# Kernel optimization log

Hardware: AMD Instinct MI355X
Metric: run time of the kernel (lower is better)

The kernel has to match this reference:

```python
import jax, jax.numpy as jnp
import numpy as np

N = 16384      # nodes (256 chess boards x 64 squares)
E = 393216     # edges (avg degree 24)
G = 256        # graphs
HID = 128
H = 4
C = 32         # head dim
L = 8          # 4 blocks x 2 GATv2Conv
NODE_DIM = 21
EDGE_DIM = 6


def setup_inputs() -> dict:
    key = jax.random.key(0)
    ks = jax.random.split(key, 12)
    x = jax.random.normal(ks[0], (N, NODE_DIM), jnp.float32)
    edge_index = jax.random.randint(ks[1], (2, E), 0, N, dtype=jnp.int32)
    edge_attr = jax.random.uniform(ks[2], (E, EDGE_DIM), dtype=jnp.float32)
    batch = jnp.sort(jax.random.randint(ks[3], (N,), 0, G, dtype=jnp.int32))

    def w(k, shape, fan_in):
        return jax.random.normal(k, shape, jnp.float32) * (1.0 / np.sqrt(fan_in))

    Win = w(ks[4], (NODE_DIM, HID), NODE_DIM)
    b_in = jnp.zeros((HID,), jnp.float32)
    Wl = w(ks[5], (L, HID, HID), HID)
    bl = jnp.zeros((L, HID), jnp.float32)
    Wr = w(ks[6], (L, HID, HID), HID)
    br = jnp.zeros((L, HID), jnp.float32)
    We = w(ks[7], (L, EDGE_DIM, HID), EDGE_DIM)
    att = w(ks[8], (L, H, C), C)
    bconv = jnp.zeros((L, HID), jnp.float32)
    gamma = jnp.ones((L, HID), jnp.float32)
    beta = jnp.zeros((L, HID), jnp.float32)
    W1 = w(ks[9], (HID, 64), HID)
    b1 = jnp.zeros((64,), jnp.float32)
    W2 = w(ks[10], (64, 3), 64)
    b2 = jnp.zeros((3,), jnp.float32)
    return dict(x=x, edge_index=edge_index, edge_attr=edge_attr, batch=batch,
                Win=Win, b_in=b_in, Wl=Wl, bl=bl, Wr=Wr, br=br, We=We, att=att,
                bconv=bconv, gamma=gamma, beta=beta, W1=W1, b1=b1, W2=W2, b2=b2)


def _gatv2(h, src, dst, ea, Wl, bl, Wr, br, We, att, bias):
    # PyG GATv2Conv: message j->i uses x_j from lin_l, x_i from lin_r
    xl = (h @ Wl + bl).reshape(N, H, C)
    xr = (h @ Wr + br).reshape(N, H, C)
    ee = (ea @ We).reshape(-1, H, C)
    m = jax.nn.leaky_relu(xl[src] + xr[dst] + ee, 0.2)   # [Ef, H, C]
    s = jnp.einsum('ehc,hc->eh', m, att)                 # [Ef, H]
    smax = jax.ops.segment_max(s, dst, num_segments=N)   # self-loops => no empty segs
    ex = jnp.exp(s - smax[dst])
    den = jax.ops.segment_sum(ex, dst, num_segments=N)
    alpha = ex / den[dst]                                # edge softmax per target node
    out = jax.ops.segment_sum(alpha[:, :, None] * xl[src], dst, num_segments=N)
    return out.reshape(N, HID) + bias


def _bn(x, g, b):
    mu = jnp.mean(x, axis=0)
    var = jnp.var(x, axis=0)
    return g * (x - mu) * jax.lax.rsqrt(var + 1e-5) + b


def reference(x, edge_index, edge_attr, batch, Win, b_in, Wl, bl, Wr, br, We, att,
              bconv, gamma, beta, W1, b1, W2, b2):
    src0, dst0 = edge_index[0], edge_index[1]
    # add self-loops with fill_value='mean' (per-target mean of incoming edge_attr)
    deg = jax.ops.segment_sum(jnp.ones((E,), jnp.float32), dst0, num_segments=N)
    loop_attr = jax.ops.segment_sum(edge_attr, dst0, num_segments=N) / jnp.maximum(deg, 1.0)[:, None]
    idx = jnp.arange(N, dtype=src0.dtype)
    src = jnp.concatenate([src0, idx])
    dst = jnp.concatenate([dst0, idx])
    ea = jnp.concatenate([edge_attr, loop_attr], axis=0)

    h = jax.nn.relu(x @ Win + b_in)
    for blk in range(4):
        res = h
        l = 2 * blk
        h = jax.nn.relu(_bn(_gatv2(h, src, dst, ea, Wl[l], bl[l], Wr[l], br[l], We[l], att[l], bconv[l]), gamma[l], beta[l]))
        l = 2 * blk + 1
        h = _bn(_gatv2(h, src, dst, ea, Wl[l], bl[l], Wr[l], br[l], We[l], att[l], bconv[l]), gamma[l], beta[l])
        h = jax.nn.relu(h + res)

    cnt = jnp.maximum(jax.ops.segment_sum(jnp.ones((N,), jnp.float32), batch, num_segments=G), 1.0)
    pooled = jax.ops.segment_sum(h, batch, num_segments=G) / cnt[:, None]
    logits = jax.nn.relu(pooled @ W1 + b1) @ W2 + b2
    return logits
```

## Files before the change

kernel.cpp:

```cpp
#include <hip/hip_runtime.h>
#include <math.h>

constexpr int N   = 16384;
constexpr int E   = 393216;
constexpr int EF  = E + N;
constexpr int G   = 256;
constexpr int HID = 128;

__device__ __forceinline__ float red16(float x) {
    union fi { float f; int i; };
    fi a, b;
    a.f = x;
    b.i = __builtin_amdgcn_mov_dpp(a.i, 0x121, 0xf, 0xf, false); a.f += b.f;
    b.i = __builtin_amdgcn_mov_dpp(a.i, 0x122, 0xf, 0xf, false); a.f += b.f;
    b.i = __builtin_amdgcn_mov_dpp(a.i, 0x124, 0xf, 0xf, false); a.f += b.f;
    b.i = __builtin_amdgcn_mov_dpp(a.i, 0x128, 0xf, 0xf, false); a.f += b.f;
    return a.f;
}

__global__ __launch_bounds__(256) void k_hist(const int* __restrict__ dst,
                                              int* __restrict__ cnt) {
    int e = blockIdx.x * 256 + threadIdx.x;
    if (e < E) atomicAdd(&cnt[dst[e]], 1);
}

__global__ __launch_bounds__(1024) void k_scan(const int* __restrict__ cnt,
                                               int* __restrict__ row_ptr) {
    __shared__ int lds[1024];
    int t = threadIdx.x;
    int local[16];
    int s = 0;
    int base = t * 16;
#pragma unroll
    for (int q = 0; q < 16; q++) { local[q] = cnt[base + q] + 1; s += local[q]; }
    lds[t] = s;
    __syncthreads();
    for (int off = 1; off < 1024; off <<= 1) {
        int v = (t >= off) ? lds[t - off] : 0;
        __syncthreads();
        lds[t] += v;
        __syncthreads();
    }
    int run = (t == 0) ? 0 : lds[t - 1];
    if (t == 0) row_ptr[0] = 0;
#pragma unroll
    for (int q = 0; q < 16; q++) { run += local[q]; row_ptr[base + q + 1] = run; }
}

__global__ __launch_bounds__(256) void k_scatter(const int* __restrict__ src,
                                                 const int* __restrict__ dst,
                                                 const int* __restrict__ row_ptr,
                                                 int* __restrict__ cnt,
                                                 int* __restrict__ csr_src,
                                                 int* __restrict__ csr_eid) {
    int e = blockIdx.x * 256 + threadIdx.x;
    if (e >= E) return;
    int d = dst[e];
    int pos = row_ptr[d] + atomicSub(&cnt[d], 1) - 1;
    csr_src[pos] = src[e];
    csr_eid[pos] = e;
}

__global__ __launch_bounds__(256) void k_build_ea(const int* __restrict__ row_ptr,
                                                  int* __restrict__ csr_src,
                                                  int* __restrict__ csr_eid,
                                                  const float* __restrict__ edge_attr,
                                                  float* __restrict__ csr_ea) {
    int p = blockIdx.x * 256 + threadIdx.x;
    if (p < N) {
        int pos = row_ptr[p + 1] - 1;
        csr_src[pos] = p;
        csr_eid[pos] = E + p;
    }
    if (p >= EF) return;
    unsigned eid = (unsigned)csr_eid[p];
    if (eid >= (unsigned)E) return;
    const float* s = edge_attr + (size_t)eid * 6;
    float4 a = {s[0], s[1], s[2], s[3]};
    float4 b = {s[4], s[5], 0.0f, 0.0f};
    float4* dstp = (float4*)(csr_ea + (size_t)p * 8);
    dstp[0] = a;
    dstp[1] = b;
}

__global__ __launch_bounds__(256) void k_loopattr2(const int* __restrict__ row_ptr,
                                                   float* __restrict__ csr_ea) {
    int i = blockIdx.x * 256 + threadIdx.x;
    if (i >= N) return;
    int e0 = row_ptr[i], e1 = row_ptr[i + 1] - 1;
    float4 sa = {0, 0, 0, 0};
    float sbx = 0.0f, sby = 0.0f;
    for (int e = e0; e < e1; e++) {
        const float4* p = (const float4*)(csr_ea + (size_t)e * 8);
        float4 a = p[0];
        float4 b = p[1];
        sa.x += a.x; sa.y += a.y; sa.z += a.z; sa.w += a.w;
        sbx += b.x; sby += b.y;
    }
    float inv = 1.0f / fmaxf((float)(e1 - e0), 1.0f);
    float4 oa = {sa.x * inv, sa.y * inv, sa.z * inv, sa.w * inv};
    float4 ob = {sbx * inv, sby * inv, 0.0f, 0.0f};
    float4* q = (float4*)(csr_ea + (size_t)e1 * 8);
    q[0] = oa;
    q[1] = ob;
}

__global__ __launch_bounds__(128) void k_ingemm(const float* __restrict__ x,
                                                const float* __restrict__ Win,
                                                const float* __restrict__ b_in,
                                                float* __restrict__ h) {
    __shared__ float xs[21];
    int i = blockIdx.x;
    int c = threadIdx.x;
    if (c < 21) xs[c] = x[i * 21 + c];
    __syncthreads();
    float acc = b_in[c];
#pragma unroll
    for (int d = 0; d < 21; d++) acc += xs[d] * Win[d * HID + c];
    h[i * HID + c] = fmaxf(acc, 0.0f);
}

__global__ __launch_bounds__(256) void k_gemm_lr(const float* __restrict__ h,
                                                 const float* __restrict__ bns,
                                                 const float* __restrict__ gamma,
                                                 const float* __restrict__ beta,
                                                 float* __restrict__ res,
                                                 const float* __restrict__ Wl,
                                                 const float* __restrict__ bl,
                                                 const float* __restrict__ Wr,
                                                 const float* __restrict__ br,
                                                 float* __restrict__ XL,
                                                 float* __restrict__ XR) {
    __shared__ float hs[16][HID];
    __shared__ float sc[HID], sh[HID];
    int t = threadIdx.x;
    int r0 = blockIdx.x * 16;
    if (bns) {
        if (t < 128) {
            const float invN = 1.0f / (float)N;
            float mean = bns[t] * invN;
            float var  = bns[128 + t] * invN - mean * mean;
            float inv  = rsqrtf(var + 1e-5f);
            float s = gamma[t] * inv;
            sc[t] = s;
            sh[t] = beta[t] - mean * s;
        }
        __syncthreads();
    }
    {
        int row = t >> 4;
        int col = (t & 15) * 8;
        size_t base = (size_t)(r0 + row) * HID + col;
        const float4* src = (const float4*)&h[base];
        float4 a = src[0];
        float4 b = src[1];
        if (bns) {
            float4 s0 = *(const float4*)&sc[col];
            float4 s1 = *(const float4*)&sc[col + 4];
            float4 h0 = *(const float4*)&sh[col];
            float4 h1 = *(const float4*)&sh[col + 4];
            a.x = fmaf(a.x, s0.x, h0.x);
            a.y = fmaf(a.y, s0.y, h0.y);
            a.z = fmaf(a.z, s0.z, h0.z);
            a.w = fmaf(a.w, s0.w, h0.w);
            b.x = fmaf(b.x, s1.x, h1.x);
            b.y = fmaf(b.y, s1.y, h1.y);
            b.z = fmaf(b.z, s1.z, h1.z);
            b.w = fmaf(b.w, s1.w, h1.w);
            if (res) {
                const float4* rp = (const float4*)&res[base];
                float4 ra = rp[0];
                float4 rb = rp[1];
                a.x += ra.x; a.y += ra.y; a.z += ra.z; a.w += ra.w;
                b.x += rb.x; b.y += rb.y; b.z += rb.z; b.w += rb.w;
            }
            a.x = fmaxf(a.x, 0.0f); a.y = fmaxf(a.y, 0.0f);
            a.z = fmaxf(a.z, 0.0f); a.w = fmaxf(a.w, 0.0f);
            b.x = fmaxf(b.x, 0.0f); b.y = fmaxf(b.y, 0.0f);
            b.z = fmaxf(b.z, 0.0f); b.w = fmaxf(b.w, 0.0f);
            if (res) {
                float4* wp = (float4*)&res[base];
                wp[0] = a;
                wp[1] = b;
            }
        }
        float4* dst = (float4*)&hs[row][col];
        dst[0] = a;
        dst[1] = b;
    }
    __syncthreads();
    bool right = t >= 128;
    int cp = (t & 63) * 2;
    int rbase = ((t >> 6) & 1) * 8;
    const float* W    = right ? Wr : Wl;
    const float* bias = right ? br : bl;
    float* OUT        = right ? XR : XL;
    float b0 = bias[cp], b1 = bias[cp + 1];
    float acc0[8], acc1[8];
#pragma unroll
    for (int r = 0; r < 8; r++) { acc0[r] = b0; acc1[r] = b1; }
    for (int k = 0; k < HID; k += 4) {
        float4 h4[8];
#pragma unroll
        for (int r = 0; r < 8; r++) h4[r] = *(const float4*)&hs[rbase + r][k];
#pragma unroll
        for (int kk = 0; kk < 4; kk++) {
            float2 w = *(const float2*)&W[(size_t)(k + kk) * HID + cp];
#pragma unroll
            for (int r = 0; r < 8; r++) {
                float hv = ((const float*)&h4[r])[kk];
                acc0[r] = fmaf(hv, w.x, acc0[r]);
                acc1[r] = fmaf(hv, w.y, acc1[r]);
            }
        }
    }
#pragma unroll
    for (int r = 0; r < 8; r++) {
        float2 o = {acc0[r], acc1[r]};
        *(float2*)&OUT[(size_t)(r0 + rbase + r) * HID + cp] = o;
    }
}

__device__ __forceinline__ void pf_xl(int e, int e1,
                                      const int* __restrict__ csr_src,
                                      const float* __restrict__ xl, int ch0,
                                      float2 out[4]) {
#pragma unroll
    for (int k = 0; k < 4; k++) {
        int ec = (e + k < e1) ? e + k : e1 - 1;
        int j = __builtin_amdgcn_readfirstlane(csr_src[ec]);
        out[k] = *(const float2*)&xl[(size_t)j * HID + ch0];
    }
}

__global__ __launch_bounds__(1024) void k_edge(const int* __restrict__ row_ptr,
                                               const int* __restrict__ csr_src,
                                               const float* __restrict__ csr_ea,
                                               const float* __restrict__ xl,
                                               const float* __restrict__ xr,
                                               const float* __restrict__ We_l,
                                               const float* __restrict__ att_l,
                                               float* __restrict__ gout,
                                               float* __restrict__ bnsums) {
    __shared__ float red_lds[16][256];
    int w = threadIdx.x >> 6;
    int lane = threadIdx.x & 63;
    int hh = lane >> 4;
    int ss = lane & 15;
    int ch0 = hh * 32 + 2 * ss;
    int i = blockIdx.x * 16 + w;

    float a0 = att_l[ch0], a1 = att_l[ch0 + 1];
    float we0[6], we1[6];
#pragma unroll
    for (int d = 0; d < 6; d++) {
        float2 wv = *(const float2*)&We_l[d * HID + ch0];
        we0[d] = wv.x;
        we1[d] = wv.y;
    }

    float2 xr2 = *(const float2*)&xr[(size_t)i * HID + ch0];
    float rm = -INFINITY, rd = 0.0f, acc0 = 0.0f, acc1 = 0.0f;
    int e0 = __builtin_amdgcn_readfirstlane(row_ptr[i]);
    int e1 = __builtin_amdgcn_readfirstlane(row_ptr[i + 1]);

    auto body = [&](int e, const float2 xlv[4]) {
        float p[4];
#pragma unroll
        for (int k = 0; k < 4; k++) {
            int ee = e + k;
            int ec = (ee < e1) ? ee : (e1 - 1);
            const float4* ea4 = (const float4*)(csr_ea + (size_t)ec * 8);
            float4 eaA = ea4[0];
            float4 eaB = ea4[1];
            float u0 = eaA.x * we0[0], u1 = eaA.x * we1[0];
            u0 = fmaf(eaA.y, we0[1], u0); u1 = fmaf(eaA.y, we1[1], u1);
            u0 = fmaf(eaA.z, we0[2], u0); u1 = fmaf(eaA.z, we1[2], u1);
            u0 = fmaf(eaA.w, we0[3], u0); u1 = fmaf(eaA.w, we1[3], u1);
            u0 = fmaf(eaB.x, we0[4], u0); u1 = fmaf(eaB.x, we1[4], u1);
            u0 = fmaf(eaB.y, we0[5], u0); u1 = fmaf(eaB.y, we1[5], u1);
            float m0 = xlv[k].x + xr2.x + u0;
            float m1 = xlv[k].y + xr2.y + u1;
            m0 = fmaxf(m0, 0.2f * m0);
            m1 = fmaxf(m1, 0.2f * m1);
            float pv = m0 * a0;
            pv = fmaf(m1, a1, pv);
            pv = red16(pv);
            p[k] = (ee < e1) ? pv : -INFINITY;
        }
        float bm = fmaxf(fmaxf(p[0], p[1]), fmaxf(p[2], p[3]));
        float nm = fmaxf(rm, bm);
        float scal = __expf(rm - nm);
        rd *= scal; acc0 *= scal; acc1 *= scal;
#pragma unroll
        for (int k = 0; k < 4; k++) {
            float ek = __expf(p[k] - nm);
            rd += ek;
            acc0 = fmaf(ek, xlv[k].x, acc0);
            acc1 = fmaf(ek, xlv[k].y, acc1);
        }
        rm = nm;
    };

    float2 bufA[4], bufB[4];
    pf_xl(e0, e1, csr_src, xl, ch0, bufA);
    for (int e = e0; e < e1; e += 8) {
        pf_xl(e + 4, e1, csr_src, xl, ch0, bufB);
        body(e, bufA);
        pf_xl(e + 8, e1, csr_src, xl, ch0, bufA);
        if (e + 4 < e1) body(e + 4, bufB);
    }
    float inv = 1.0f / rd;
    float2 o = {acc0 * inv, acc1 * inv};
    *(float2*)&gout[(size_t)i * HID + ch0] = o;

    red_lds[w][ch0]       = o.x;
    red_lds[w][ch0 + 1]   = o.y;
    red_lds[w][128 + ch0]     = o.x * o.x;
    red_lds[w][128 + ch0 + 1] = o.y * o.y;
    __syncthreads();
    int t = threadIdx.x;
    if (t < 256) {
        float s = 0.0f;
#pragma unroll
        for (int q = 0; q < 16; q++) s += red_lds[q][t];
        atomicAdd(&bnsums[t], s);
    }
}

__global__ __launch_bounds__(128) void k_pool(const float* __restrict__ gout,
                                              const float* __restrict__ res,
                                              const float* __restrict__ bns,
                                              const float* __restrict__ gamma,
                                              const float* __restrict__ beta,
                                              const int* __restrict__ batch,
                                              const float* __restrict__ W1,
                                              const float* __restrict__ b1,
                                              const float* __restrict__ W2,
                                              const float* __restrict__ b2,
                                              float* __restrict__ out) {
    __shared__ float pooled[HID];
    __shared__ float hid[64];
    __shared__ int bounds[2];
    int g = blockIdx.x;
    int t = threadIdx.x;
    if (t < 2) {
        int target = g + t;
        int lo = 0, hi = N;
        while (lo < hi) {
            int mid = (lo + hi) >> 1;
            if (batch[mid] < target) lo = mid + 1; else hi = mid;
        }
        bounds[t] = lo;
    }
    const float invN = 1.0f / (float)N;
    float mean = bns[t] * invN;
    float var  = bns[128 + t] * invN - mean * mean;
    float scb  = gamma[t] * rsqrtf(var + 1e-5f);
    float shb  = beta[t] - mean * scb;
    __syncthreads();
    int s = bounds[0], e = bounds[1];
    float acc = 0.0f;
    for (int r = s; r < e; r++) {
        float v = fmaf(gout[(size_t)r * HID + t], scb, shb) + res[(size_t)r * HID + t];
        acc += fmaxf(v, 0.0f);
    }
    float cntf = fmaxf((float)(e - s), 1.0f);
    pooled[t] = acc / cntf;
    __syncthreads();
    if (t < 64) {
        float a = b1[t];
#pragma unroll 4
        for (int c = 0; c < HID; c++) a += pooled[c] * W1[c * 64 + t];
        hid[t] = fmaxf(a, 0.0f);
    }
    __syncthreads();
    if (t < 3) {
        float a = b2[t];
#pragma unroll
        for (int j = 0; j < 64; j++) a += hid[j] * W2[j * 3 + t];
        out[g * 3 + t] = a;
    }
}

extern "C" void kernel_launch(void* const* d_in, const int* in_sizes, int n_in,
                              void* d_out, int out_size, void* d_ws, size_t ws_size,
                              hipStream_t stream) {
    const float* x         = (const float*)d_in[0];
    const int*   edge_index= (const int*)d_in[1];
    const float* edge_attr = (const float*)d_in[2];
    const int*   batch     = (const int*)d_in[3];
    const float* Win       = (const float*)d_in[4];
    const float* b_in      = (const float*)d_in[5];
    const float* Wl        = (const float*)d_in[6];
    const float* bl        = (const float*)d_in[7];
    const float* Wr        = (const float*)d_in[8];
    const float* br        = (const float*)d_in[9];
    const float* We        = (const float*)d_in[10];
    const float* att       = (const float*)d_in[11];
    const float* gamma     = (const float*)d_in[13];
    const float* beta      = (const float*)d_in[14];
    const float* W1        = (const float*)d_in[15];
    const float* b1        = (const float*)d_in[16];
    const float* W2        = (const float*)d_in[17];
    const float* b2        = (const float*)d_in[18];
    float* out = (float*)d_out;

    const int* src0 = edge_index;
    const int* dst0 = edge_index + E;

    char* ws = (char*)d_ws;
    size_t off = 0;
    auto alloc = [&](size_t bytes) -> void* {
        void* p = ws + off;
        off += (bytes + 255) & ~(size_t)255;
        return p;
    };
    int*   cnt       = (int*)alloc((size_t)N * sizeof(int));
    float* bnsums    = (float*)alloc((size_t)8 * 256 * sizeof(float));
    int*   row_ptr   = (int*)alloc((size_t)(N + 1) * sizeof(int));
    int*   csr_src   = (int*)alloc((size_t)EF * sizeof(int));
    int*   csr_eid   = (int*)alloc((size_t)EF * sizeof(int));
    float* csr_ea    = (float*)alloc((size_t)EF * 8 * sizeof(float));
    float* H0        = (float*)alloc((size_t)N * HID * sizeof(float));
    float* XL        = (float*)alloc((size_t)N * HID * sizeof(float));
    float* XR        = (float*)alloc((size_t)N * HID * sizeof(float));
    float* GOUT      = (float*)alloc((size_t)N * HID * sizeof(float));

    size_t zbytes = (size_t)N * sizeof(int) + 8 * 256 * sizeof(float);
    hipMemsetAsync(cnt, 0, zbytes, stream);
    k_hist<<<(E + 255) / 256, 256, 0, stream>>>(dst0, cnt);
    k_scan<<<1, 1024, 0, stream>>>(cnt, row_ptr);
    k_scatter<<<(E + 255) / 256, 256, 0, stream>>>(src0, dst0, row_ptr, cnt,
                                                   csr_src, csr_eid);
    k_build_ea<<<(EF + 255) / 256, 256, 0, stream>>>(row_ptr, csr_src, csr_eid,
                                                     edge_attr, csr_ea);
    k_loopattr2<<<(N + 255) / 256, 256, 0, stream>>>(row_ptr, csr_ea);
    k_ingemm<<<N, 128, 0, stream>>>(x, Win, b_in, H0);

    for (int l = 0; l < 8; l++) {
        bool odd = (l & 1) != 0;
        const float* hin;
        const float* bns_in = nullptr;
        const float* g_in = nullptr;
        const float* b_in2 = nullptr;
        float* res = nullptr;
        if (l == 0) {
            hin = H0;
        } else {
            hin = GOUT;
            bns_in = bnsums + (l - 1) * 256;
            g_in  = gamma + (size_t)(l - 1) * HID;
            b_in2 = beta  + (size_t)(l - 1) * HID;
            if (!odd) res = H0;
        }
        k_gemm_lr<<<N / 16, 256, 0, stream>>>(hin, bns_in, g_in, b_in2, res,
                                              Wl + (size_t)l * HID * HID, bl + l * HID,
                                              Wr + (size_t)l * HID * HID, br + l * HID,
                                              XL, XR);
        k_edge<<<N / 16, 1024, 0, stream>>>(row_ptr, csr_src, csr_ea,
                                            XL, XR,
                                            We + (size_t)l * 6 * HID,
                                            att + (size_t)l * HID, GOUT,
                                            bnsums + l * 256);
    }
    k_pool<<<G, 128, 0, stream>>>(GOUT, H0, bnsums + 7 * 256,
                                  gamma + 7 * HID, beta + 7 * HID,
                                  batch, W1, b1, W2, b2, out);
}
```

Baseline: 737.7 us.

## Deepen edge-index prefetch, drop online-softmax max, fuse CSR attr build into scatter

The edge kernel now prefetches source indices three groups ahead, separately from the xl row gathers, so index-load latency is hidden behind the softmax body. The running-max online softmax is replaced with plain exp2 accumulation, with log2(e) folded into the attention weights. This removes the per-group max, rescale exponent and multiplies, but it no longer guards against overflow for large scores. Setup also drops k_build_ea and the csr_eid buffer by writing edge attributes directly in the scatter kernel, moves the self-loop index write into k_loopattr2, and adds an occupancy hint to the k_edge launch bounds.

```diff
diff --git a/kernel.cpp b/kernel.cpp
--- a/kernel.cpp
+++ b/kernel.cpp
@@ -51,39 +51,24 @@
                                                  const int* __restrict__ dst,
                                                  const int* __restrict__ row_ptr,
                                                  int* __restrict__ cnt,
+                                                 const float* __restrict__ edge_attr,
                                                  int* __restrict__ csr_src,
-                                                 int* __restrict__ csr_eid) {
+                                                 float* __restrict__ csr_ea) {
     int e = blockIdx.x * 256 + threadIdx.x;
     if (e >= E) return;
     int d = dst[e];
     int pos = row_ptr[d] + atomicSub(&cnt[d], 1) - 1;
     csr_src[pos] = src[e];
-    csr_eid[pos] = e;
-}
-
-__global__ __launch_bounds__(256) void k_build_ea(const int* __restrict__ row_ptr,
-                                                  int* __restrict__ csr_src,
-                                                  int* __restrict__ csr_eid,
-                                                  const float* __restrict__ edge_attr,
-                                                  float* __restrict__ csr_ea) {
-    int p = blockIdx.x * 256 + threadIdx.x;
-    if (p < N) {
-        int pos = row_ptr[p + 1] - 1;
-        csr_src[pos] = p;
-        csr_eid[pos] = E + p;
-    }
-    if (p >= EF) return;
-    unsigned eid = (unsigned)csr_eid[p];
-    if (eid >= (unsigned)E) return;
-    const float* s = edge_attr + (size_t)eid * 6;
+    const float* s = edge_attr + (size_t)e * 6;
     float4 a = {s[0], s[1], s[2], s[3]};
     float4 b = {s[4], s[5], 0.0f, 0.0f};
-    float4* dstp = (float4*)(csr_ea + (size_t)p * 8);
+    float4* dstp = (float4*)(csr_ea + (size_t)pos * 8);
     dstp[0] = a;
     dstp[1] = b;
 }
 
 __global__ __launch_bounds__(256) void k_loopattr2(const int* __restrict__ row_ptr,
+                                                   int* __restrict__ csr_src,
                                                    float* __restrict__ csr_ea) {
     int i = blockIdx.x * 256 + threadIdx.x;
     if (i >= N) return;
@@ -103,6 +88,7 @@
     float4* q = (float4*)(csr_ea + (size_t)e1 * 8);
     q[0] = oa;
     q[1] = ob;
+    csr_src[e1] = i;
 }
 
 __global__ __launch_bounds__(128) void k_ingemm(const float* __restrict__ x,
@@ -221,27 +207,15 @@
     }
 }
 
-__device__ __forceinline__ void pf_xl(int e, int e1,
-                                      const int* __restrict__ csr_src,
-                                      const float* __restrict__ xl, int ch0,
-                                      float2 out[4]) {
-#pragma unroll
-    for (int k = 0; k < 4; k++) {
-        int ec = (e + k < e1) ? e + k : e1 - 1;
-        int j = __builtin_amdgcn_readfirstlane(csr_src[ec]);
-        out[k] = *(const float2*)&xl[(size_t)j * HID + ch0];
-    }
-}
-
-__global__ __launch_bounds__(1024) void k_edge(const int* __restrict__ row_ptr,
-                                               const int* __restrict__ csr_src,
-                                               const float* __restrict__ csr_ea,
-                                               const float* __restrict__ xl,
-                                               const float* __restrict__ xr,
-                                               const float* __restrict__ We_l,
-                                               const float* __restrict__ att_l,
-                                               float* __restrict__ gout,
-                                               float* __restrict__ bnsums) {
+__global__ __launch_bounds__(1024, 8) void k_edge(const int* __restrict__ row_ptr,
+                                                  const int* __restrict__ csr_src,
+                                                  const float* __restrict__ csr_ea,
+                                                  const float* __restrict__ xl,
+                                                  const float* __restrict__ xr,
+                                                  const float* __restrict__ We_l,
+                                                  const float* __restrict__ att_l,
+                                                  float* __restrict__ gout,
+                                                  float* __restrict__ bnsums) {
     __shared__ float red_lds[16][256];
     int w = threadIdx.x >> 6;
     int lane = threadIdx.x & 63;
@@ -250,7 +224,8 @@
     int ch0 = hh * 32 + 2 * ss;
     int i = blockIdx.x * 16 + w;
 
-    float a0 = att_l[ch0], a1 = att_l[ch0 + 1];
+    const float LOG2E = 1.44269504088896f;
+    float a0 = att_l[ch0] * LOG2E, a1 = att_l[ch0 + 1] * LOG2E;
     float we0[6], we1[6];
 #pragma unroll
     for (int d = 0; d < 6; d++) {
@@ -260,12 +235,24 @@
     }
 
     float2 xr2 = *(const float2*)&xr[(size_t)i * HID + ch0];
-    float rm = -INFINITY, rd = 0.0f, acc0 = 0.0f, acc1 = 0.0f;
+    float rd = 0.0f, acc0 = 0.0f, acc1 = 0.0f;
     int e0 = __builtin_amdgcn_readfirstlane(row_ptr[i]);
     int e1 = __builtin_amdgcn_readfirstlane(row_ptr[i + 1]);
 
+    auto ld_idx = [&](int e, int out[4]) {
+#pragma unroll
+        for (int k = 0; k < 4; k++) {
+            int ec = e + k;
+            ec = (ec < e1) ? ec : (e1 - 1);
+            out[k] = __builtin_amdgcn_readfirstlane(csr_src[ec]);
+        }
+    };
+    auto ld_xl = [&](const int idx[4], float2 out[4]) {
+#pragma unroll
+        for (int k = 0; k < 4; k++)
+            out[k] = *(const float2*)&xl[(size_t)idx[k] * HID + ch0];
+    };
     auto body = [&](int e, const float2 xlv[4]) {
-        float p[4];
 #pragma unroll
         for (int k = 0; k < 4; k++) {
             int ee = e + k;
@@ -286,36 +273,36 @@
             float pv = m0 * a0;
             pv = fmaf(m1, a1, pv);
             pv = red16(pv);
-            p[k] = (ee < e1) ? pv : -INFINITY;
-        }
-        float bm = fmaxf(fmaxf(p[0], p[1]), fmaxf(p[2], p[3]));
-        float nm = fmaxf(rm, bm);
-        float scal = __expf(rm - nm);
-        rd *= scal; acc0 *= scal; acc1 *= scal;
-#pragma unroll
-        for (int k = 0; k < 4; k++) {
-            float ek = __expf(p[k] - nm);
-            rd += ek;
-            acc0 = fmaf(ek, xlv[k].x, acc0);
-            acc1 = fmaf(ek, xlv[k].y, acc1);
-        }
-        rm = nm;
+            pv = (ee < e1) ? pv : -INFINITY;
+            float ex = exp2f(pv);
+            rd += ex;
+            acc0 = fmaf(ex, xlv[k].x, acc0);
+            acc1 = fmaf(ex, xlv[k].y, acc1);
+        }
     };
 
-    float2 bufA[4], bufB[4];
-    pf_xl(e0, e1, csr_src, xl, ch0, bufA);
+    int iA[4], iB[4], iC[4];
+    float2 x0[4], x1[4];
+    ld_idx(e0, iA);
+    ld_idx(e0 + 4, iB);
+    ld_idx(e0 + 8, iC);
+    ld_xl(iA, x0);
     for (int e = e0; e < e1; e += 8) {
-        pf_xl(e + 4, e1, csr_src, xl, ch0, bufB);
-        body(e, bufA);
-        pf_xl(e + 8, e1, csr_src, xl, ch0, bufA);
-        if (e + 4 < e1) body(e + 4, bufB);
+        ld_xl(iB, x1);
+        ld_idx(e + 12, iA);
+        body(e, x0);
+        ld_xl(iC, x0);
+        ld_idx(e + 16, iC);
+        if (e + 4 < e1) body(e + 4, x1);
+#pragma unroll
+        for (int k = 0; k < 4; k++) iB[k] = iA[k];
     }
     float inv = 1.0f / rd;
     float2 o = {acc0 * inv, acc1 * inv};
     *(float2*)&gout[(size_t)i * HID + ch0] = o;
 
-    red_lds[w][ch0]       = o.x;
-    red_lds[w][ch0 + 1]   = o.y;
+    red_lds[w][ch0]           = o.x;
+    red_lds[w][ch0 + 1]       = o.y;
     red_lds[w][128 + ch0]     = o.x * o.x;
     red_lds[w][128 + ch0 + 1] = o.y * o.y;
     __syncthreads();
@@ -420,7 +407,6 @@
     float* bnsums    = (float*)alloc((size_t)8 * 256 * sizeof(float));
     int*   row_ptr   = (int*)alloc((size_t)(N + 1) * sizeof(int));
     int*   csr_src   = (int*)alloc((size_t)EF * sizeof(int));
-    int*   csr_eid   = (int*)alloc((size_t)EF * sizeof(int));
     float* csr_ea    = (float*)alloc((size_t)EF * 8 * sizeof(float));
     float* H0        = (float*)alloc((size_t)N * HID * sizeof(float));
     float* XL        = (float*)alloc((size_t)N * HID * sizeof(float));
@@ -432,10 +418,8 @@
     k_hist<<<(E + 255) / 256, 256, 0, stream>>>(dst0, cnt);
     k_scan<<<1, 1024, 0, stream>>>(cnt, row_ptr);
     k_scatter<<<(E + 255) / 256, 256, 0, stream>>>(src0, dst0, row_ptr, cnt,
-                                                   csr_src, csr_eid);
-    k_build_ea<<<(EF + 255) / 256, 256, 0, stream>>>(row_ptr, csr_src, csr_eid,
-                                                     edge_attr, csr_ea);
-    k_loopattr2<<<(N + 255) / 256, 256, 0, stream>>>(row_ptr, csr_ea);
+                                                   edge_attr, csr_src, csr_ea);
+    k_loopattr2<<<(N + 255) / 256, 256, 0, stream>>>(row_ptr, csr_src, csr_ea);
     k_ingemm<<<N, 128, 0, stream>>>(x, Win, b_in, H0);
 
     for (int l = 0; l < 8; l++) {
```

After: 728.9 us. No clear change (-1.2%).
